# Kernel optimization log

Measured on AMD Instinct MI355X. Metric: run time of the kernel, lower is better.

The kernel has to match this reference:

```python
import jax, jax.numpy as jnp
import numpy as np

IN_FEATURES = 4096
OUT_FEATURES = 4096
KERNEL_SIZE = 4  # MaxPool1d stride defaults to kernel_size
SCALE = 0.5


def setup_inputs() -> dict:
    key = jax.random.key(0)
    kx, kw, kb = jax.random.split(key, 3)
    bound = 1.0 / np.sqrt(IN_FEATURES)
    x = jax.random.normal(kx, (4096, IN_FEATURES), dtype=jnp.float32)
    W = jax.random.uniform(kw, (OUT_FEATURES, IN_FEATURES), dtype=jnp.float32, minval=-bound, maxval=bound)
    b = jax.random.uniform(kb, (OUT_FEATURES,), dtype=jnp.float32, minval=-bound, maxval=bound)
    return {"x": x, "W": W, "b": b}


def reference(x, W, b) -> jnp.ndarray:
    # Linear: [B, I] @ [I, O] + [O] -> [B, O]
    y = jnp.einsum("bi,oi->bo", x, W) + b
    B, O = y.shape
    K = KERNEL_SIZE
    n_win = (O - K) // K + 1  # stride == kernel_size, no padding
    # Non-overlapping window max-pool: [B, n_win, K] -> max over K
    pooled = y[:, : n_win * K].reshape(B, n_win, K).max(axis=-1)
    # Sum over pooled dim, then scale -> [B]
    return pooled.sum(axis=-1) * SCALE
```

## Files before the change

### kernel.cpp

```cpp
#include <hip/hip_runtime.h>
#include <hip/hip_bf16.h>

#define KDIM 4096
#define NTILE 64
#define NELEM16 (1u << 24)

typedef float f32x4 __attribute__((ext_vector_type(4)));
typedef short bf16x8 __attribute__((ext_vector_type(8)));

typedef const __attribute__((address_space(1))) unsigned int g_u32;
typedef __attribute__((address_space(3))) unsigned int l_u32;

__device__ __forceinline__ void gload_lds16(const void* g, void* l) {
    __builtin_amdgcn_global_load_lds((g_u32*)g, (l_u32*)l, 16, 0, 0);
}

__device__ __forceinline__ unsigned int pack_bf16x2(float lo, float hi) {
    __hip_bfloat162 h = __float22bfloat162_rn(float2{lo, hi});
    union { __hip_bfloat162 h; unsigned int u; } c; c.h = h; return c.u;
}

__global__ __launch_bounds__(256)
void pack_swz2(const float* __restrict__ x, const float* __restrict__ W,
               unsigned short* __restrict__ xb, unsigned short* __restrict__ wb)
{
    const unsigned int stride = gridDim.x * blockDim.x;
    for (unsigned int i = blockIdx.x * blockDim.x + threadIdx.x; i < (1u << 22); i += stride) {
        const unsigned int j  = i & ((1u << 21) - 1);
        const float* __restrict__ in = (i >> 21) ? W : x;
        unsigned short* __restrict__ out = (i >> 21) ? wb : xb;
        const unsigned int cp = j & 7;
        const unsigned int rl = (j >> 3) & 127;
        const unsigned int c  = cp ^ (rl & 7);
        const unsigned int h  = (j >> 10) & 1;
        const unsigned int kt = (j >> 11) & 63;
        const unsigned int rt = j >> 17;
        const unsigned int row = rt * 256 + h * 128 + rl;
        const unsigned int col = kt * 64 + c * 8;
        const float4* s = (const float4*)(in + (size_t)row * KDIM + col);
        const float4 a = s[0], b = s[1];
        uint4 o;
        o.x = pack_bf16x2(a.x, a.y); o.y = pack_bf16x2(a.z, a.w);
        o.z = pack_bf16x2(b.x, b.y); o.w = pack_bf16x2(b.z, b.w);
        *(uint4*)(out + (size_t)j * 8) = o;
    }
}

#define STAGE(matBase, kt, h, bufn, opIdx)                                      \
    {                                                                           \
        const unsigned short* g_ = (matBase) + ((size_t)(kt) * 2 + (h)) * 8192; \
        const unsigned int lo_ = (bufn) * 32768 + (opIdx) * 16384 + (h) * 8192 + wid * 1024; \
        gload_lds16(g_ + stageOff,       &lds[lo_]);                            \
        gload_lds16(g_ + stageOff + 512, &lds[lo_ + 512]);                      \
    }

#define READ_A(dst, base)                                                       \
    _Pragma("unroll") for (int m = 0; m < 4; ++m)                               \
      _Pragma("unroll") for (int k = 0; k < 2; ++k)                             \
        dst[m][k] = *(const bf16x8*)&lds[(base) + (m * 2 + wm) * 1024 + rdBase + kcp[k]];

#define READ_B(dst, base)                                                       \
    _Pragma("unroll") for (int n = 0; n < 2; ++n)                               \
      _Pragma("unroll") for (int k = 0; k < 2; ++k)                             \
        dst[n][k] = *(const bf16x8*)&lds[(base) + (n * 4 + wn) * 1024 + rdBase + kcp[k]];

#define MFMA16(AF, BF, MO, NO)                                                  \
    __builtin_amdgcn_s_setprio(1);                                              \
    _Pragma("unroll") for (int m = 0; m < 4; ++m)                               \
      _Pragma("unroll") for (int n = 0; n < 2; ++n)                             \
        _Pragma("unroll") for (int k = 0; k < 2; ++k)                           \
          acc[(MO) + m][(NO) + n] = __builtin_amdgcn_mfma_f32_16x16x32_bf16(    \
              AF[m][k], BF[n][k], acc[(MO) + m][(NO) + n], 0, 0, 0);            \
    __builtin_amdgcn_s_setprio(0);

#define TILE_BODY(t, PB, BUFN)                                                  \
    {                                                                           \
                                        \
        READ_A(afr, (PB));                                                      \
        READ_B(b0, (PB) + 16384);                                               \
        if ((t) + 1 < NTILE) {                                                  \
            STAGE(Abase, (t) + 1, 0, BUFN, 0);                                  \
            STAGE(Bbase, (t) + 1, 0, BUFN, 1);                                  \
            asm volatile("s_waitcnt vmcnt(4)" ::: "memory");                    \
        } else {                                                                \
            asm volatile("s_waitcnt vmcnt(0)" ::: "memory");                    \
        }                                                                       \
        __builtin_amdgcn_s_barrier();                                           \
        __builtin_amdgcn_sched_barrier(0);                                      \
        MFMA16(afr, b0, 0, 0);                                                  \
        READ_B(b1, (PB) + 16384 + 8192);                                        \
        MFMA16(afr, b1, 0, 2);                                                  \
                                        \
        READ_A(afr, (PB) + 8192);                                               \
        if ((t) + 1 < NTILE) {                                                  \
            STAGE(Bbase, (t) + 1, 1, BUFN, 1);                                  \
            STAGE(Abase, (t) + 1, 1, BUFN, 0);                                  \
            asm volatile("s_waitcnt vmcnt(4)" ::: "memory");                    \
        } else {                                                                \
            asm volatile("s_waitcnt vmcnt(0)" ::: "memory");                    \
        }                                                                       \
        __builtin_amdgcn_s_barrier();                                           \
        __builtin_amdgcn_sched_barrier(0);                                      \
        MFMA16(afr, b1, 4, 2);                                                  \
        MFMA16(afr, b0, 4, 0);                                                  \
    }

__global__ __launch_bounds__(512, 2)
void gemm_8phase(const unsigned short* __restrict__ A,
                 const unsigned short* __restrict__ B,
                 const float* __restrict__ bias,
                 float* __restrict__ out)
{
    __shared__ unsigned short lds[65536];

    const int tid  = threadIdx.x;
    const int lane = tid & 63;
    const int wid  = tid >> 6;
    const int wm   = wid >> 2;
    const int wn   = wid & 3;
    const int c15  = lane & 15;
    const int q4   = lane >> 4;
    const int c7   = c15 & 7;

    const int bid = blockIdx.x;
    const int wg  = (bid & 7) * 32 + (bid >> 3);
    const int bm  = wg >> 4;
    const int bn  = wg & 15;

    const unsigned short* Abase = A + (size_t)bm * 64 * 2 * 8192;
    const unsigned short* Bbase = B + (size_t)bn * 64 * 2 * 8192;

    const int stageOff = wid * 1024 + lane * 8;
    const int rdBase   = c15 * 64;
    const int kcp[2]   = { ((0 + q4) ^ c7) * 8, ((4 + q4) ^ c7) * 8 };

    f32x4 acc[8][4];
    #pragma unroll
    for (int i = 0; i < 8; ++i)
        #pragma unroll
        for (int j = 0; j < 4; ++j)
            acc[i][j] = (f32x4)0.0f;

    bf16x8 afr[4][2];
    bf16x8 b0[2][2];
    bf16x8 b1[2][2];

    STAGE(Abase, 0, 0, 0, 0);
    STAGE(Bbase, 0, 0, 0, 1);
    STAGE(Bbase, 0, 1, 0, 1);
    STAGE(Abase, 0, 1, 0, 0);
    asm volatile("s_waitcnt vmcnt(4)" ::: "memory");
    __builtin_amdgcn_s_barrier();
    __builtin_amdgcn_sched_barrier(0);

    for (int tt = 0; tt < NTILE; tt += 2) {
        TILE_BODY(tt,     0,     1);
        TILE_BODY(tt + 1, 32768, 0);
    }

    float rs[8][4];
    #pragma unroll
    for (int mf = 0; mf < 8; ++mf)
        #pragma unroll
        for (int r = 0; r < 4; ++r)
            rs[mf][r] = 0.0f;

    #pragma unroll
    for (int nf = 0; nf < 4; ++nf) {
        const float bv = bias[bn * 256 + (nf * 4 + wn) * 16 + c15];
        #pragma unroll
        for (int mf = 0; mf < 8; ++mf) {
            #pragma unroll
            for (int r = 0; r < 4; ++r) {
                float v = acc[mf][nf][r] + bv;
                v = fmaxf(v, __shfl_xor(v, 1));
                v = fmaxf(v, __shfl_xor(v, 2));
                v += __shfl_xor(v, 4);
                v += __shfl_xor(v, 8);
                rs[mf][r] += v;
            }
        }
    }

    if (c15 == 0) {
        #pragma unroll
        for (int mf = 0; mf < 8; ++mf)
            #pragma unroll
            for (int r = 0; r < 4; ++r) {
                const int row = bm * 256 + (mf * 2 + wm) * 16 + q4 * 4 + r;
                atomicAdd(&out[row], 0.5f * rs[mf][r]);
            }
    }
}

__global__ __launch_bounds__(256, 2)
void fused_gemm_pool_fallback(const float* __restrict__ x,
                              const float* __restrict__ W,
                              const float* __restrict__ b,
                              float* __restrict__ out)
{
    __shared__ unsigned short As[128][72];
    __shared__ unsigned short Bs[128][72];

    const int tid  = threadIdx.x;
    const int lane = tid & 63;
    const int wid  = tid >> 6;
    const int wm   = wid >> 1;
    const int wn   = wid & 1;

    const int bid = blockIdx.x;
    const int wg  = (bid & 7) * 128 + (bid >> 3);
    const int bm  = wg >> 5;
    const int bn  = wg & 31;

    const int srow = tid >> 4;
    const int scol = tid & 15;

    const float* xbase = x + (size_t)(bm * 128 + srow) * KDIM + scol * 4;
    const float* wbase = W + (size_t)(bn * 128 + srow) * KDIM + scol * 4;

    f32x4 acc[4][4];
    #pragma unroll
    for (int i = 0; i < 4; ++i)
        #pragma unroll
        for (int j = 0; j < 4; ++j)
            acc[i][j] = (f32x4)0.0f;

    float4 ra[8], rb[8];
    #pragma unroll
    for (int p = 0; p < 8; ++p) {
        ra[p] = *(const float4*)(xbase + (size_t)(p * 16) * KDIM);
        rb[p] = *(const float4*)(wbase + (size_t)(p * 16) * KDIM);
    }

    for (int kt = 0; kt < KDIM / 64; ++kt) {
        #pragma unroll
        for (int p = 0; p < 8; ++p) {
            const int r = srow + p * 16;
            uint2 pa, pb;
            pa.x = pack_bf16x2(ra[p].x, ra[p].y);
            pa.y = pack_bf16x2(ra[p].z, ra[p].w);
            pb.x = pack_bf16x2(rb[p].x, rb[p].y);
            pb.y = pack_bf16x2(rb[p].z, rb[p].w);
            *(uint2*)&As[r][scol * 4] = pa;
            *(uint2*)&Bs[r][scol * 4] = pb;
        }
        __syncthreads();

        if (kt + 1 < KDIM / 64) {
            const float* xa = xbase + (size_t)(kt + 1) * 64;
            const float* wa = wbase + (size_t)(kt + 1) * 64;
            #pragma unroll
            for (int p = 0; p < 8; ++p) {
                ra[p] = *(const float4*)(xa + (size_t)(p * 16) * KDIM);
                rb[p] = *(const float4*)(wa + (size_t)(p * 16) * KDIM);
            }
        }

        #pragma unroll
        for (int k0 = 0; k0 < 2; ++k0) {
            const int kk = k0 * 32 + (lane >> 4) * 8;
            bf16x8 af[4], bfr[4];
            #pragma unroll
            for (int mf = 0; mf < 4; ++mf)
                af[mf] = *(const bf16x8*)&As[wm * 64 + mf * 16 + (lane & 15)][kk];
            #pragma unroll
            for (int nf = 0; nf < 4; ++nf)
                bfr[nf] = *(const bf16x8*)&Bs[wn * 64 + nf * 16 + (lane & 15)][kk];
            #pragma unroll
            for (int mf = 0; mf < 4; ++mf)
                #pragma unroll
                for (int nf = 0; nf < 4; ++nf)
                    acc[mf][nf] = __builtin_amdgcn_mfma_f32_16x16x32_bf16(
                        af[mf], bfr[nf], acc[mf][nf], 0, 0, 0);
        }
        __syncthreads();
    }

    float rs[4][4];
    #pragma unroll
    for (int mf = 0; mf < 4; ++mf)
        #pragma unroll
        for (int r = 0; r < 4; ++r)
            rs[mf][r] = 0.0f;

    #pragma unroll
    for (int nf = 0; nf < 4; ++nf) {
        const float bv = b[bn * 128 + wn * 64 + nf * 16 + (lane & 15)];
        #pragma unroll
        for (int mf = 0; mf < 4; ++mf) {
            #pragma unroll
            for (int r = 0; r < 4; ++r) {
                float v = acc[mf][nf][r] + bv;
                v = fmaxf(v, __shfl_xor(v, 1));
                v = fmaxf(v, __shfl_xor(v, 2));
                v += __shfl_xor(v, 4);
                v += __shfl_xor(v, 8);
                rs[mf][r] += v;
            }
        }
    }

    if ((lane & 15) == 0) {
        #pragma unroll
        for (int mf = 0; mf < 4; ++mf)
            #pragma unroll
            for (int r = 0; r < 4; ++r) {
                const int row = bm * 128 + wm * 64 + mf * 16 + (lane >> 4) * 4 + r;
                atomicAdd(&out[row], 0.5f * rs[mf][r]);
            }
    }
}

extern "C" void kernel_launch(void* const* d_in, const int* in_sizes, int n_in,
                              void* d_out, int out_size, void* d_ws, size_t ws_size,
                              hipStream_t stream) {
    const float* x = (const float*)d_in[0];
    const float* W = (const float*)d_in[1];
    const float* b = (const float*)d_in[2];
    float* out = (float*)d_out;

    hipMemsetAsync(out, 0, (size_t)out_size * sizeof(float), stream);

    const size_t need = (size_t)NELEM16 * 2 * sizeof(unsigned short);
    if (ws_size >= need) {
        unsigned short* xb = (unsigned short*)d_ws;
        unsigned short* wb = xb + (size_t)NELEM16;
        pack_swz2<<<dim3(2048), dim3(256), 0, stream>>>(x, W, xb, wb);
        gemm_8phase<<<dim3(256), dim3(512), 0, stream>>>(xb, wb, b, out);
    } else {
        fused_gemm_pool_fallback<<<dim3(1024), dim3(256), 0, stream>>>(x, W, b, out);
    }
}
```

Measured before the change: 164.4 us.

## Load B operand directly from global into registers, bypassing LDS

The pack kernel now writes W in an MFMA-fragment-ready layout, so each lane can load its B fragments straight from global memory into registers. The GEMM loop double-buffers those fragments in registers and stages only A through LDS, which halves LDS use. This removes B LDS writes and reads plus the related bank traffic. In exchange it raises register pressure (launch bounds drop to one block per SM slot) and depends on global-load latency being hidden by the register double buffer.

```diff
diff --git a/kernel.cpp b/kernel.cpp
--- a/kernel.cpp
+++ b/kernel.cpp
@@ -21,35 +21,48 @@
 }
 
 __global__ __launch_bounds__(256)
-void pack_swz2(const float* __restrict__ x, const float* __restrict__ W,
-               unsigned short* __restrict__ xb, unsigned short* __restrict__ wb)
+void pack2(const float* __restrict__ x, const float* __restrict__ W,
+           unsigned short* __restrict__ xb, unsigned short* __restrict__ wb)
 {
     const unsigned int stride = gridDim.x * blockDim.x;
     for (unsigned int i = blockIdx.x * blockDim.x + threadIdx.x; i < (1u << 22); i += stride) {
-        const unsigned int j  = i & ((1u << 21) - 1);
-        const float* __restrict__ in = (i >> 21) ? W : x;
-        unsigned short* __restrict__ out = (i >> 21) ? wb : xb;
-        const unsigned int cp = j & 7;
-        const unsigned int rl = (j >> 3) & 127;
-        const unsigned int c  = cp ^ (rl & 7);
-        const unsigned int h  = (j >> 10) & 1;
-        const unsigned int kt = (j >> 11) & 63;
-        const unsigned int rt = j >> 17;
-        const unsigned int row = rt * 256 + h * 128 + rl;
-        const unsigned int col = kt * 64 + c * 8;
-        const float4* s = (const float4*)(in + (size_t)row * KDIM + col);
-        const float4 a = s[0], b = s[1];
+        const float* __restrict__ in;
+        unsigned short* __restrict__ out;
+        unsigned int row, col, E;
+        if (i < (1u << 21)) {
+            const unsigned int cp = i & 7;
+            const unsigned int rl = (i >> 3) & 127;
+            const unsigned int c  = cp ^ (rl & 7);
+            const unsigned int h  = (i >> 10) & 1;
+            const unsigned int kt = (i >> 11) & 63;
+            const unsigned int rt = i >> 17;
+            row = rt * 256 + h * 128 + rl;
+            col = kt * 64 + c * 8;
+            in = x; out = xb; E = i * 8;
+        } else {
+            const unsigned int j    = i - (1u << 21);
+            const unsigned int lane = j & 63;
+            const unsigned int s    = (j >> 6) & 1;
+            const unsigned int cf   = (j >> 7) & 15;
+            const unsigned int kt   = (j >> 11) & 63;
+            const unsigned int ot   = j >> 17;
+            row = ot * 256 + cf * 16 + (lane & 15);
+            col = kt * 64 + s * 32 + (lane >> 4) * 8;
+            in = W; out = wb; E = j * 8;
+        }
+        const float4* sp = (const float4*)(in + (size_t)row * KDIM + col);
+        const float4 a = sp[0], b = sp[1];
         uint4 o;
         o.x = pack_bf16x2(a.x, a.y); o.y = pack_bf16x2(a.z, a.w);
         o.z = pack_bf16x2(b.x, b.y); o.w = pack_bf16x2(b.z, b.w);
-        *(uint4*)(out + (size_t)j * 8) = o;
-    }
-}
-
-#define STAGE(matBase, kt, h, bufn, opIdx)                                      \
+        *(uint4*)(out + (size_t)E) = o;
+    }
+}
+
+#define STAGE_A(kt, h, bufn)                                                    \
     {                                                                           \
-        const unsigned short* g_ = (matBase) + ((size_t)(kt) * 2 + (h)) * 8192; \
-        const unsigned int lo_ = (bufn) * 32768 + (opIdx) * 16384 + (h) * 8192 + wid * 1024; \
+        const unsigned short* g_ = Abase + ((size_t)(kt) * 2 + (h)) * 8192;     \
+        const unsigned int lo_ = (bufn) * 16384 + (h) * 8192 + wid * 1024;      \
         gload_lds16(g_ + stageOff,       &lds[lo_]);                            \
         gload_lds16(g_ + stageOff + 512, &lds[lo_ + 512]);                      \
     }
@@ -59,59 +72,73 @@
       _Pragma("unroll") for (int k = 0; k < 2; ++k)                             \
         dst[m][k] = *(const bf16x8*)&lds[(base) + (m * 2 + wm) * 1024 + rdBase + kcp[k]];
 
-#define READ_B(dst, base)                                                       \
+#define LOAD_B(dst, t, nbase)                                                   \
     _Pragma("unroll") for (int n = 0; n < 2; ++n)                               \
-      _Pragma("unroll") for (int k = 0; k < 2; ++k)                             \
-        dst[n][k] = *(const bf16x8*)&lds[(base) + (n * 4 + wn) * 1024 + rdBase + kcp[k]];
-
-#define MFMA16(AF, BF, MO, NO)                                                  \
+      _Pragma("unroll") for (int s = 0; s < 2; ++s)                             \
+        dst[n][s] = *(const bf16x8*)&Bbase[(size_t)(t) * 16384 +                \
+            ((((nbase) + n) * 4 + wn) * 2 + s) * 512 + lane * 8];
+
+#define MFMA32(AF, BF0, BF1, MO)                                                \
     __builtin_amdgcn_s_setprio(1);                                              \
     _Pragma("unroll") for (int m = 0; m < 4; ++m)                               \
       _Pragma("unroll") for (int n = 0; n < 2; ++n)                             \
         _Pragma("unroll") for (int k = 0; k < 2; ++k)                           \
-          acc[(MO) + m][(NO) + n] = __builtin_amdgcn_mfma_f32_16x16x32_bf16(    \
-              AF[m][k], BF[n][k], acc[(MO) + m][(NO) + n], 0, 0, 0);            \
+          acc[(MO) + m][n] = __builtin_amdgcn_mfma_f32_16x16x32_bf16(           \
+              AF[m][k], BF0[n][k], acc[(MO) + m][n], 0, 0, 0);                  \
+    _Pragma("unroll") for (int m = 0; m < 4; ++m)                               \
+      _Pragma("unroll") for (int n = 0; n < 2; ++n)                             \
+        _Pragma("unroll") for (int k = 0; k < 2; ++k)                           \
+          acc[(MO) + m][2 + n] = __builtin_amdgcn_mfma_f32_16x16x32_bf16(       \
+              AF[m][k], BF1[n][k], acc[(MO) + m][2 + n], 0, 0, 0);              \
     __builtin_amdgcn_s_setprio(0);
 
-#define TILE_BODY(t, PB, BUFN)                                                  \
+#define TILE_BODY(t, PB, BUFN, C0, C1, N0, N1)                                  \
     {                                                                           \
-                                        \
         READ_A(afr, (PB));                                                      \
-        READ_B(b0, (PB) + 16384);                                               \
         if ((t) + 1 < NTILE) {                                                  \
-            STAGE(Abase, (t) + 1, 0, BUFN, 0);                                  \
-            STAGE(Bbase, (t) + 1, 0, BUFN, 1);                                  \
-            asm volatile("s_waitcnt vmcnt(4)" ::: "memory");                    \
+            STAGE_A((t) + 1, 0, BUFN);                                          \
+            LOAD_B(N0, (t) + 1, 0);                                             \
+            asm volatile("s_waitcnt vmcnt(6)" ::: "memory");                    \
         } else {                                                                \
             asm volatile("s_waitcnt vmcnt(0)" ::: "memory");                    \
         }                                                                       \
         __builtin_amdgcn_s_barrier();                                           \
         __builtin_amdgcn_sched_barrier(0);                                      \
-        MFMA16(afr, b0, 0, 0);                                                  \
-        READ_B(b1, (PB) + 16384 + 8192);                                        \
-        MFMA16(afr, b1, 0, 2);                                                  \
-                                        \
+        MFMA32(afr, C0, C1, 0);                                                 \
         READ_A(afr, (PB) + 8192);                                               \
         if ((t) + 1 < NTILE) {                                                  \
-            STAGE(Bbase, (t) + 1, 1, BUFN, 1);                                  \
-            STAGE(Abase, (t) + 1, 1, BUFN, 0);                                  \
-            asm volatile("s_waitcnt vmcnt(4)" ::: "memory");                    \
+            STAGE_A((t) + 1, 1, BUFN);                                          \
+            LOAD_B(N1, (t) + 1, 2);                                             \
+            asm volatile("s_waitcnt vmcnt(6)" ::: "memory");                    \
         } else {                                                                \
             asm volatile("s_waitcnt vmcnt(0)" ::: "memory");                    \
         }                                                                       \
         __builtin_amdgcn_s_barrier();                                           \
         __builtin_amdgcn_sched_barrier(0);                                      \
-        MFMA16(afr, b1, 4, 2);                                                  \
-        MFMA16(afr, b0, 4, 0);                                                  \
-    }
-
-__global__ __launch_bounds__(512, 2)
-void gemm_8phase(const unsigned short* __restrict__ A,
-                 const unsigned short* __restrict__ B,
-                 const float* __restrict__ bias,
-                 float* __restrict__ out)
+        MFMA32R(afr, C1, C0, 4);                                                \
+    }
+
+#define MFMA32R(AF, BF1, BF0, MO)                                               \
+    __builtin_amdgcn_s_setprio(1);                                              \
+    _Pragma("unroll") for (int m = 0; m < 4; ++m)                               \
+      _Pragma("unroll") for (int n = 0; n < 2; ++n)                             \
+        _Pragma("unroll") for (int k = 0; k < 2; ++k)                           \
+          acc[(MO) + m][2 + n] = __builtin_amdgcn_mfma_f32_16x16x32_bf16(       \
+              AF[m][k], BF1[n][k], acc[(MO) + m][2 + n], 0, 0, 0);              \
+    _Pragma("unroll") for (int m = 0; m < 4; ++m)                               \
+      _Pragma("unroll") for (int n = 0; n < 2; ++n)                             \
+        _Pragma("unroll") for (int k = 0; k < 2; ++k)                           \
+          acc[(MO) + m][n] = __builtin_amdgcn_mfma_f32_16x16x32_bf16(           \
+              AF[m][k], BF0[n][k], acc[(MO) + m][n], 0, 0, 0);                  \
+    __builtin_amdgcn_s_setprio(0);
+
+__global__ __launch_bounds__(512, 1)
+void gemm_bdirect(const unsigned short* __restrict__ A,
+                  const unsigned short* __restrict__ B,
+                  const float* __restrict__ bias,
+                  float* __restrict__ out)
 {
-    __shared__ unsigned short lds[65536];
+    __shared__ unsigned short lds[32768];
 
     const int tid  = threadIdx.x;
     const int lane = tid & 63;
@@ -128,7 +155,7 @@
     const int bn  = wg & 15;
 
     const unsigned short* Abase = A + (size_t)bm * 64 * 2 * 8192;
-    const unsigned short* Bbase = B + (size_t)bn * 64 * 2 * 8192;
+    const unsigned short* Bbase = B + ((size_t)bn << 20);
 
     const int stageOff = wid * 1024 + lane * 8;
     const int rdBase   = c15 * 64;
@@ -142,20 +169,20 @@
             acc[i][j] = (f32x4)0.0f;
 
     bf16x8 afr[4][2];
-    bf16x8 b0[2][2];
-    bf16x8 b1[2][2];
-
-    STAGE(Abase, 0, 0, 0, 0);
-    STAGE(Bbase, 0, 0, 0, 1);
-    STAGE(Bbase, 0, 1, 0, 1);
-    STAGE(Abase, 0, 1, 0, 0);
-    asm volatile("s_waitcnt vmcnt(4)" ::: "memory");
+    bf16x8 bE0[2][2], bE1[2][2];
+    bf16x8 bO0[2][2], bO1[2][2];
+
+    STAGE_A(0, 0, 0);
+    STAGE_A(0, 1, 0);
+    LOAD_B(bE0, 0, 0);
+    LOAD_B(bE1, 0, 2);
+    asm volatile("s_waitcnt vmcnt(8)" ::: "memory");
     __builtin_amdgcn_s_barrier();
     __builtin_amdgcn_sched_barrier(0);
 
     for (int tt = 0; tt < NTILE; tt += 2) {
-        TILE_BODY(tt,     0,     1);
-        TILE_BODY(tt + 1, 32768, 0);
+        TILE_BODY(tt,     0,     1, bE0, bE1, bO0, bO1);
+        TILE_BODY(tt + 1, 16384, 0, bO0, bO1, bE0, bE1);
     }
 
     float rs[8][4];
@@ -326,8 +353,8 @@
     if (ws_size >= need) {
         unsigned short* xb = (unsigned short*)d_ws;
         unsigned short* wb = xb + (size_t)NELEM16;
-        pack_swz2<<<dim3(2048), dim3(256), 0, stream>>>(x, W, xb, wb);
-        gemm_8phase<<<dim3(256), dim3(512), 0, stream>>>(xb, wb, b, out);
+        pack2<<<dim3(2048), dim3(256), 0, stream>>>(x, W, xb, wb);
+        gemm_bdirect<<<dim3(256), dim3(512), 0, stream>>>(xb, wb, b, out);
     } else {
         fused_gemm_pool_fallback<<<dim3(1024), dim3(256), 0, stream>>>(x, W, b, out);
     }
```

Measured after the change: 164.6 us. About the same (+0.1%).

## Restructure GEMM main loop into eight-phase pipeline with deeper prefetch

Applied to the files above, without the earlier changes.

Replaces the two-half tile body with an eight-phase schedule. Each phase issues one half-operand staging load, does one MFMA block and has barriers on both sides, and global loads now run up to two tiles ahead with vmcnt(6) waits. Prefetching deeper and spreading loads evenly across compute phases is meant to hide global-to-LDS latency better. It adds more barriers per tile and changes launch bounds from two blocks to one per CU, which may reduce occupancy.

```diff
diff --git a/kernel.cpp b/kernel.cpp
--- a/kernel.cpp
+++ b/kernel.cpp
@@ -64,48 +64,55 @@
       _Pragma("unroll") for (int k = 0; k < 2; ++k)                             \
         dst[n][k] = *(const bf16x8*)&lds[(base) + (n * 4 + wn) * 1024 + rdBase + kcp[k]];
 
-#define MFMA16(AF, BF, MO, NO)                                                  \
-    __builtin_amdgcn_s_setprio(1);                                              \
-    _Pragma("unroll") for (int m = 0; m < 4; ++m)                               \
-      _Pragma("unroll") for (int n = 0; n < 2; ++n)                             \
-        _Pragma("unroll") for (int k = 0; k < 2; ++k)                           \
-          acc[(MO) + m][(NO) + n] = __builtin_amdgcn_mfma_f32_16x16x32_bf16(    \
-              AF[m][k], BF[n][k], acc[(MO) + m][(NO) + n], 0, 0, 0);            \
-    __builtin_amdgcn_s_setprio(0);
-
-#define TILE_BODY(t, PB, BUFN)                                                  \
+#define PHASE(RDS, STG, AF, BF, MO, NO, VMW)                                    \
     {                                                                           \
-                                        \
-        READ_A(afr, (PB));                                                      \
-        READ_B(b0, (PB) + 16384);                                               \
-        if ((t) + 1 < NTILE) {                                                  \
-            STAGE(Abase, (t) + 1, 0, BUFN, 0);                                  \
-            STAGE(Bbase, (t) + 1, 0, BUFN, 1);                                  \
-            asm volatile("s_waitcnt vmcnt(4)" ::: "memory");                    \
-        } else {                                                                \
-            asm volatile("s_waitcnt vmcnt(0)" ::: "memory");                    \
-        }                                                                       \
+        RDS;                                                                    \
+        STG;                                                                    \
         __builtin_amdgcn_s_barrier();                                           \
-        __builtin_amdgcn_sched_barrier(0);                                      \
-        MFMA16(afr, b0, 0, 0);                                                  \
-        READ_B(b1, (PB) + 16384 + 8192);                                        \
-        MFMA16(afr, b1, 0, 2);                                                  \
-                                        \
-        READ_A(afr, (PB) + 8192);                                               \
-        if ((t) + 1 < NTILE) {                                                  \
-            STAGE(Bbase, (t) + 1, 1, BUFN, 1);                                  \
-            STAGE(Abase, (t) + 1, 1, BUFN, 0);                                  \
-            asm volatile("s_waitcnt vmcnt(4)" ::: "memory");                    \
-        } else {                                                                \
-            asm volatile("s_waitcnt vmcnt(0)" ::: "memory");                    \
-        }                                                                       \
+        __builtin_amdgcn_s_setprio(1);                                          \
+        _Pragma("unroll") for (int m = 0; m < 4; ++m)                           \
+          _Pragma("unroll") for (int n = 0; n < 2; ++n)                         \
+            _Pragma("unroll") for (int k = 0; k < 2; ++k)                       \
+              acc[(MO) + m][(NO) + n] = __builtin_amdgcn_mfma_f32_16x16x32_bf16(\
+                  AF[m][k], BF[n][k], acc[(MO) + m][(NO) + n], 0, 0, 0);        \
+        __builtin_amdgcn_s_setprio(0);                                          \
+        VMW;                                                                    \
         __builtin_amdgcn_s_barrier();                                           \
-        __builtin_amdgcn_sched_barrier(0);                                      \
-        MFMA16(afr, b1, 4, 2);                                                  \
-        MFMA16(afr, b0, 4, 0);                                                  \
-    }
-
-__global__ __launch_bounds__(512, 2)
+    }
+
+#define VM6 asm volatile("s_waitcnt vmcnt(6)" ::: "memory")
+#define VM0 asm volatile("s_waitcnt vmcnt(0)" ::: "memory")
+
+#define ITER(t)                                                                 \
+    PHASE(READ_A(afr, 0); READ_B(b0, 16384),                                    \
+          STAGE(Abase, (t)+1, 1, 1, 0), afr, b0, 0, 0, )                        \
+    PHASE(READ_B(b1, 16384 + 8192),                                             \
+          STAGE(Abase, (t)+2, 0, 0, 0), afr, b1, 0, 2, )                        \
+    PHASE(READ_A(afr, 8192),                                                    \
+          STAGE(Bbase, (t)+2, 0, 0, 1), afr, b1, 4, 2, )                        \
+    PHASE(,                                                                     \
+          STAGE(Bbase, (t)+2, 1, 0, 1), afr, b0, 4, 0, VM6)                     \
+    PHASE(READ_A(afr, 32768); READ_B(b0, 32768 + 16384),                        \
+          STAGE(Abase, (t)+2, 1, 0, 0), afr, b0, 0, 0, )                        \
+    PHASE(READ_B(b1, 32768 + 16384 + 8192),                                     \
+          STAGE(Abase, (t)+3, 0, 1, 0), afr, b1, 0, 2, )                        \
+    PHASE(READ_A(afr, 32768 + 8192),                                            \
+          STAGE(Bbase, (t)+3, 0, 1, 1), afr, b1, 4, 2, )                        \
+    PHASE(,                                                                     \
+          STAGE(Bbase, (t)+3, 1, 1, 1), afr, b0, 4, 0, VM6)
+
+#define ITER_LAST()                                                             \
+    PHASE(READ_A(afr, 0); READ_B(b0, 16384),                                    \
+          STAGE(Abase, 63, 1, 1, 0), afr, b0, 0, 0, )                           \
+    PHASE(READ_B(b1, 16384 + 8192), , afr, b1, 0, 2, )                          \
+    PHASE(READ_A(afr, 8192), , afr, b1, 4, 2, )                                 \
+    PHASE(, , afr, b0, 4, 0, VM0)                                               \
+    PHASE(READ_A(afr, 32768); READ_B(b0, 32768 + 16384), , afr, b0, 0, 0, )     \
+    PHASE(READ_B(b1, 32768 + 16384 + 8192), , afr, b1, 0, 2, )                  \
+    PHASE(READ_A(afr, 32768 + 8192), , afr, b1, 4, 2, )                         \
+    PHASE(, , afr, b0, 4, 0, )
+
+__global__ __launch_bounds__(512, 1)
 void gemm_8phase(const unsigned short* __restrict__ A,
                  const unsigned short* __restrict__ B,
                  const float* __restrict__ bias,
@@ -127,8 +134,8 @@
     const int bm  = wg >> 4;
     const int bn  = wg & 15;
 
-    const unsigned short* Abase = A + (size_t)bm * 64 * 2 * 8192;
-    const unsigned short* Bbase = B + (size_t)bn * 64 * 2 * 8192;
+    const unsigned short* Abase = A + ((size_t)bm << 20);
+    const unsigned short* Bbase = B + ((size_t)bn << 20);
 
     const int stageOff = wid * 1024 + lane * 8;
     const int rdBase   = c15 * 64;
@@ -149,14 +156,16 @@
     STAGE(Bbase, 0, 0, 0, 1);
     STAGE(Bbase, 0, 1, 0, 1);
     STAGE(Abase, 0, 1, 0, 0);
-    asm volatile("s_waitcnt vmcnt(4)" ::: "memory");
+    STAGE(Abase, 1, 0, 1, 0);
+    STAGE(Bbase, 1, 0, 1, 1);
+    STAGE(Bbase, 1, 1, 1, 1);
+    VM6;
     __builtin_amdgcn_s_barrier();
-    __builtin_amdgcn_sched_barrier(0);
-
-    for (int tt = 0; tt < NTILE; tt += 2) {
-        TILE_BODY(tt,     0,     1);
-        TILE_BODY(tt + 1, 32768, 0);
-    }
+
+    for (int t = 0; t < 62; t += 2) {
+        ITER(t)
+    }
+    ITER_LAST()
 
     float rs[8][4];
     #pragma unroll
```

Measured after the change: 167.8 us. +2.1%, slower.
